# Optimization experiments

Measured on AMD Instinct MI355X. Metric: run time of the kernel, lower is better.

The kernel has to match this reference:

```python
import jax, jax.numpy as jnp
import numpy as np


def _gru_layer(x, w_ih, w_hh, b_ih, b_hh):
    """PyTorch-semantics GRU over x:[B,T,I]. w_ih:[3H,I], w_hh:[3H,H]."""
    B, T, I = x.shape
    H = w_hh.shape[1]
    # precompute input-side gates for all timesteps: [T,B,3H]
    gx = (jnp.einsum('bti,gi->btg', x, w_ih) + b_ih).transpose(1, 0, 2)

    def step(h, gx_t):
        gh = h @ w_hh.T + b_hh  # [B,3H]
        xr, xz, xn = jnp.split(gx_t, 3, axis=-1)
        hr, hz, hn = jnp.split(gh, 3, axis=-1)
        r = jax.nn.sigmoid(xr + hr)
        z = jax.nn.sigmoid(xz + hz)
        n = jnp.tanh(xn + r * hn)
        h_new = (1.0 - z) * n + z * h
        return h_new, h_new

    h0 = jnp.zeros((B, H), dtype=x.dtype)
    _, hs = jax.lax.scan(step, h0, gx)  # hs: [T,B,H]
    return hs.transpose(1, 0, 2)


def _gru_params(key, in_size, hidden):
    k = 1.0 / np.sqrt(hidden)
    k1, k2, k3, k4 = jax.random.split(key, 4)
    w_ih = jax.random.uniform(k1, (3 * hidden, in_size), minval=-k, maxval=k, dtype=jnp.float32)
    w_hh = jax.random.uniform(k2, (3 * hidden, hidden), minval=-k, maxval=k, dtype=jnp.float32)
    b_ih = jax.random.uniform(k3, (3 * hidden,), minval=-k, maxval=k, dtype=jnp.float32)
    b_hh = jax.random.uniform(k4, (3 * hidden,), minval=-k, maxval=k, dtype=jnp.float32)
    return w_ih, w_hh, b_ih, b_hh


def setup_inputs() -> dict:
    key = jax.random.key(0)
    ks = jax.random.split(key, 6)
    B, T = 256, 1024
    x = jax.random.normal(ks[0], (B, T), dtype=jnp.float32)
    sizes = [(1, 256), (256, 128), (128, 128), (128, 256)]
    d = {'x': x}
    for i, (isz, h) in enumerate(sizes):
        w_ih, w_hh, b_ih, b_hh = _gru_params(ks[1 + i], isz, h)
        d[f'w_ih{i+1}'] = w_ih
        d[f'w_hh{i+1}'] = w_hh
        d[f'b_ih{i+1}'] = b_ih
        d[f'b_hh{i+1}'] = b_hh
    kw, kb = jax.random.split(ks[5])
    kk = 1.0 / np.sqrt(256.0)
    d['w_out'] = jax.random.uniform(kw, (1, 256), minval=-kk, maxval=kk, dtype=jnp.float32)
    d['b_out'] = jax.random.uniform(kb, (1,), minval=-kk, maxval=kk, dtype=jnp.float32)
    return d


def reference(x, w_ih1, w_hh1, b_ih1, b_hh1,
              w_ih2, w_hh2, b_ih2, b_hh2,
              w_ih3, w_hh3, b_ih3, b_hh3,
              w_ih4, w_hh4, b_ih4, b_hh4,
              w_out, b_out):
    h = x[..., None]  # [B,T,1]
    h = _gru_layer(h, w_ih1, w_hh1, b_ih1, b_hh1)
    h = _gru_layer(h, w_ih2, w_hh2, b_ih2, b_hh2)
    h = _gru_layer(h, w_ih3, w_hh3, b_ih3, b_hh3)
    h = _gru_layer(h, w_ih4, w_hh4, b_ih4, b_hh4)
    y = jnp.einsum('bth,oh->bto', h, w_out) + b_out  # TimeDistributed Linear(256,1)
    return y.reshape(y.shape[0], -1)  # flatten from dim 1 -> [B,T]
```

## Files before the change

### kernel.cpp

```cpp
#include <hip/hip_runtime.h>
#include <math.h>


__device__ __forceinline__ float sigmoidf_(float v) {
    return 1.0f / (1.0f + __expf(-v));
}
__device__ __forceinline__ float tanhf_(float v) {
    float e = __expf(2.0f * v);
    return 1.0f - 2.0f / (e + 1.0f);
}

__global__ void prep_k(const float* __restrict__ src, float* __restrict__ dst,
                       int H, int J) {
    int idx = blockIdx.x * 256 + threadIdx.x;
    int total = 3 * H * J;
    if (idx < total) {
        int g = idx / (H * J);
        int rem = idx - g * H * J;
        int u = rem / J;
        int j = rem - u * J;
        dst[(u * 3 + g) * J + j] = src[(g * H + u) * J + j];
    }
}


__device__ __forceinline__ void flag_st(int* p, int v) {
    __hip_atomic_store(p, v, __ATOMIC_RELAXED, __HIP_MEMORY_SCOPE_AGENT);
}
__device__ __forceinline__ int flag_ld(const int* p) {
    return __hip_atomic_load(p, __ATOMIC_RELAXED, __HIP_MEMORY_SCOPE_AGENT);
}
__device__ __forceinline__ void ex_store(float* p, float v) {
    __hip_atomic_store(p, v, __ATOMIC_RELAXED, __HIP_MEMORY_SCOPE_AGENT);
}

__device__ __forceinline__ void pollw(const int* p, int tgt, bool active,
                                      int& fc) {
    bool need = active && (fc < tgt);
    if (!__any(need)) return;
    int spins = 0;
    while (true) {
        if (need) { fc = flag_ld(p); need = (fc < tgt); }
        if (!__any(need)) return;
        if (++spins > 16) __builtin_amdgcn_s_sleep(1);
        if (spins > 200000) return;
    }
}


template <int J>
__device__ __forceinline__ void stage_load(float4* r, const float* src) {
    constexpr int NF4 = (32 * J) / 1024;
    #pragma unroll
    for (int k = 0; k < NF4; ++k) {
        const float* p = src + (size_t)(k * 256 + threadIdx.x) * 4;
        asm volatile("global_load_dwordx4 %0, %1, off sc0 sc1"
                     : "=v"(r[k]) : "v"(p) : "memory");
    }
}

template <int J>
__device__ __forceinline__ void stage_write(const float4* r, float* dst) {
    constexpr int NF4 = (32 * J) / 1024;
    constexpr int LJ = (J == 256) ? 8 : 7;
    #pragma unroll
    for (int k = 0; k < NF4; ++k) {
        int i = (k * 256 + threadIdx.x) * 4;
        int b = i >> LJ;
        int j = i & (J - 1);
        *(float4*)(dst + b * (J + 4) + j) = r[k];
    }
}

template <int J>
__device__ __forceinline__ void stageX(float* dst, const float* src) {
    float4 tmp[(32 * J) / 1024];
    stage_load<J>(tmp, src);
    asm volatile("s_waitcnt vmcnt(0)" ::: "memory");
    stage_write<J>(tmp, dst);
}

template <int J>
__device__ __forceinline__ void zero32(float* dst) {
    for (int i = threadIdx.x; i < 32 * (J + 4); i += 256) dst[i] = 0.0f;
}

template <int U, int J>
__device__ __forceinline__ void ring_store(float* hout, const float* hst) {
    constexpr int LU = (U == 32) ? 5 : 4;
    #pragma unroll
    for (int k = 0; k < (32 * U) / 256; ++k) {
        int i = k * 256 + threadIdx.x;
        int b = i >> LU;
        int c = i & (U - 1);
        ex_store(hout + b * J + c, hst[b * (U + 4) + c]);
    }
}

template <int KB, int J>
__device__ __forceinline__ void dot3(const float* __restrict__ w3,
                                     const float* __restrict__ hst, int b0,
                                     float* ar, float* az, float* ac) {
    const float4* wr = (const float4*)w3;
    const float4* wz = (const float4*)(w3 + J);
    const float4* wn = (const float4*)(w3 + 2 * J);
    const float* rows[KB];
    #pragma unroll
    for (int k = 0; k < KB; ++k) rows[k] = hst + (b0 + k * (32 / KB)) * (J + 4);
    #pragma unroll 4
    for (int j4 = 0; j4 < J / 4; ++j4) {
        float4 a = wr[j4];
        float4 c = wz[j4];
        float4 d = wn[j4];
        #pragma unroll
        for (int k = 0; k < KB; ++k) {
            float4 hv = *(const float4*)(rows[k] + j4 * 4);
            ar[k] = fmaf(hv.x, a.x, ar[k]); ar[k] = fmaf(hv.y, a.y, ar[k]);
            ar[k] = fmaf(hv.z, a.z, ar[k]); ar[k] = fmaf(hv.w, a.w, ar[k]);
            az[k] = fmaf(hv.x, c.x, az[k]); az[k] = fmaf(hv.y, c.y, az[k]);
            az[k] = fmaf(hv.z, c.z, az[k]); az[k] = fmaf(hv.w, c.w, az[k]);
            ac[k] = fmaf(hv.x, d.x, ac[k]); ac[k] = fmaf(hv.y, d.y, ac[k]);
            ac[k] = fmaf(hv.z, d.z, ac[k]); ac[k] = fmaf(hv.w, d.w, ac[k]);
        }
    }
}

__global__ __launch_bounds__(256) void gru_pipe_kernel(
    const float* __restrict__ x,
    const float* __restrict__ w_ih1,
    const float* __restrict__ b_ih1, const float* __restrict__ b_hh1,
    const float* __restrict__ b_ih2, const float* __restrict__ b_hh2,
    const float* __restrict__ b_ih3, const float* __restrict__ b_hh3,
    const float* __restrict__ b_ih4, const float* __restrict__ b_hh4,
    const float* __restrict__ wA_hh1,
    const float* __restrict__ wA_ih2,
    const float* __restrict__ wA_hh2,
    const float* __restrict__ wA_ih3,
    const float* __restrict__ wA_hh3,
    const float* __restrict__ wA_ih4,
    const float* __restrict__ wA_hh4,
    const float* __restrict__ w_out, const float* __restrict__ b_out,
    int* __restrict__ flags,
    float* __restrict__ ex,
    float* __restrict__ out)
{
    const int tid = threadIdx.x;
    const int lane = tid & 63;
    extern __shared__ float smem[];
    __shared__ float xs[32];
    __shared__ float wsum[4][4][8];

    const int bg = blockIdx.x & 7;
    const int rest = blockIdx.x >> 3;
    const int s = rest >> 3;
    const int us = rest & 7;

    int* fb = flags + bg * 128;
    int* arr_own = fb + s * 32;

    const int* pT = arr_own; int dT = 0; bool aT = false;
    const int* pM = arr_own; bool aM = false;
    if (lane < 8) {
        if (s > 0) { pT = fb + (s - 1) * 32 + lane; dT = 1; aT = true; }
        pM = arr_own + lane; aM = true;
    } else if (lane < 16) {
        if (s < 3) { pT = fb + (s + 1) * 32 + (lane - 8); dT = -3; aT = true; }
    }
    const bool aUp = (s > 0) && (lane < 8);
    int fcT = 0, fcM = 0;

    float* exb = ex + (size_t)bg * 98304;
    float* h1r = exb;
    float* h2r = exb + 32768;
    float* h3r = exb + 49152;
    float* h4r = exb + 65536;

    if (s == 0) {
        float* wlds = smem;
        float* hprev = smem + 24704;
        float* hst = smem + 33024;
        {
            const float* srcw = wA_hh1 + (size_t)us * 32 * 768;
            for (int i = tid; i < 24576; i += 256) {
                int uu = i / 768, r = i - uu * 768;
                wlds[uu * 772 + r] = srcw[i];
            }
        }
        __syncthreads();
        const int ul = tid >> 3, b0 = tid & 7;
        const int u = us * 32 + ul;
        const float* wh = wlds + ul * 772;
        const float br = b_ih1[u] + b_hh1[u];
        const float bz = b_ih1[u + 256] + b_hh1[u + 256];
        const float bxn = b_ih1[u + 512];
        const float bhn = b_hh1[u + 512];
        const float wir = w_ih1[u], wiz = w_ih1[u + 256], win = w_ih1[u + 512];
        for (int t = 0; t < 1024; ++t) {
            pollw(pT, t + dT, aT, fcT);
            if (tid < 32) xs[tid] = x[(size_t)(bg * 32 + tid) * 1024 + t];
            pollw(pM, t, aM, fcM);
            if (t > 0) stageX<256>(hprev, h1r + (size_t)((t - 1) & 3) * 8192);
            else       zero32<256>(hprev);
            __syncthreads();
            float ar[4], az[4], axn[4], ahn[4];
            #pragma unroll
            for (int k = 0; k < 4; ++k) {
                float xv = xs[b0 + 8 * k];
                ar[k] = br + xv * wir; az[k] = bz + xv * wiz;
                axn[k] = bxn + xv * win; ahn[k] = bhn;
            }
            dot3<4, 256>(wh, hprev, b0, ar, az, ahn);
            float* hout = h1r + (size_t)(t & 3) * 8192;
            #pragma unroll
            for (int k = 0; k < 4; ++k) {
                int b = b0 + 8 * k;
                float hp = hprev[b * 260 + u];
                float r = sigmoidf_(ar[k]);
                float z = sigmoidf_(az[k]);
                float n = tanhf_(axn[k] + r * ahn[k]);
                hst[b * 36 + ul] = (1.f - z) * n + z * hp;
            }
            __syncthreads();
            ring_store<32, 256>(hout + us * 32, hst);
            asm volatile("s_waitcnt vmcnt(0)" ::: "memory");
            __syncthreads();
            if (tid == 0) flag_st(arr_own + us, t + 1);
        }
    } else if (s == 1) {
        float* wlds = smem;
        float* hin = smem + 6208;
        float* hprev = smem + 14528;
        float* hst = smem + 18752;
        {
            const float* srcw = wA_hh2 + (size_t)us * 16 * 384;
            for (int i = tid; i < 6144; i += 256) {
                int uu = i / 384, r = i - uu * 384;
                wlds[uu * 388 + r] = srcw[i];
            }
        }
        __syncthreads();
        const int ul = tid >> 4, b0 = tid & 15;
        const int u = us * 16 + ul;
        const float* wi = wA_ih2 + (size_t)u * 768;
        const float* wh = wlds + ul * 388;
        const float br = b_ih2[u] + b_hh2[u];
        const float bz = b_ih2[u + 128] + b_hh2[u + 128];
        const float bxn = b_ih2[u + 256];
        const float bhn = b_hh2[u + 256];
        float4 pregs[8];
        bool pf = false;
        for (int t = 0; t < 1024; ++t) {
            pollw(pT, t + dT, aT && (lane >= 8 || !pf), fcT);
            if (pf) stage_write<256>(pregs, hin);
            else    stageX<256>(hin, h1r + (size_t)(t & 3) * 8192);
            __syncthreads();
            float ar[2] = {br, br}, az[2] = {bz, bz};
            float axn[2] = {bxn, bxn}, ahn[2] = {bhn, bhn};
            dot3<2, 256>(wi, hin, b0, ar, az, axn);
            pollw(pM, t, aM, fcM);
            if (t > 0) stageX<128>(hprev, h2r + (size_t)((t - 1) & 3) * 4096);
            else       zero32<128>(hprev);
            __syncthreads();
            dot3<2, 128>(wh, hprev, b0, ar, az, ahn);
            pf = false;
            if (t < 1023) {
                if (aUp && fcT < t + 2) fcT = flag_ld(pT);
                pf = __all(!aUp || fcT >= t + 2);
                if (pf) stage_load<256>(pregs, h1r + (size_t)((t + 1) & 3) * 8192);
            }
            float* hout = h2r + (size_t)(t & 3) * 4096;
            #pragma unroll
            for (int k = 0; k < 2; ++k) {
                int b = b0 + 16 * k;
                float hp = hprev[b * 132 + u];
                float r = sigmoidf_(ar[k]);
                float z = sigmoidf_(az[k]);
                float n = tanhf_(axn[k] + r * ahn[k]);
                hst[b * 20 + ul] = (1.f - z) * n + z * hp;
            }
            __syncthreads();
            ring_store<16, 128>(hout + us * 16, hst);
            asm volatile("s_waitcnt vmcnt(0)" ::: "memory");
            __syncthreads();
            if (tid == 0) flag_st(arr_own + us, t + 1);
        }
    } else if (s == 2) {
        float* wlds = smem;
        float* hin = smem + 6208;
        float* hprev = smem + 10432;
        float* hst = smem + 14656;
        {
            const float* srcw = wA_hh3 + (size_t)us * 16 * 384;
            for (int i = tid; i < 6144; i += 256) {
                int uu = i / 384, r = i - uu * 384;
                wlds[uu * 388 + r] = srcw[i];
            }
        }
        __syncthreads();
        const int ul = tid >> 4, b0 = tid & 15;
        const int u = us * 16 + ul;
        const float* wi = wA_ih3 + (size_t)u * 384;
        const float* wh = wlds + ul * 388;
        const float br = b_ih3[u] + b_hh3[u];
        const float bz = b_ih3[u + 128] + b_hh3[u + 128];
        const float bxn = b_ih3[u + 256];
        const float bhn = b_hh3[u + 256];
        float4 pregs[4];
        bool pf = false;
        for (int t = 0; t < 1024; ++t) {
            pollw(pT, t + dT, aT && (lane >= 8 || !pf), fcT);
            if (pf) stage_write<128>(pregs, hin);
            else    stageX<128>(hin, h2r + (size_t)(t & 3) * 4096);
            __syncthreads();
            float ar[2] = {br, br}, az[2] = {bz, bz};
            float axn[2] = {bxn, bxn}, ahn[2] = {bhn, bhn};
            dot3<2, 128>(wi, hin, b0, ar, az, axn);
            pollw(pM, t, aM, fcM);
            if (t > 0) stageX<128>(hprev, h3r + (size_t)((t - 1) & 3) * 4096);
            else       zero32<128>(hprev);
            __syncthreads();
            dot3<2, 128>(wh, hprev, b0, ar, az, ahn);
            pf = false;
            if (t < 1023) {
                if (aUp && fcT < t + 2) fcT = flag_ld(pT);
                pf = __all(!aUp || fcT >= t + 2);
                if (pf) stage_load<128>(pregs, h2r + (size_t)((t + 1) & 3) * 4096);
            }
            float* hout = h3r + (size_t)(t & 3) * 4096;
            #pragma unroll
            for (int k = 0; k < 2; ++k) {
                int b = b0 + 16 * k;
                float hp = hprev[b * 132 + u];
                float r = sigmoidf_(ar[k]);
                float z = sigmoidf_(az[k]);
                float n = tanhf_(axn[k] + r * ahn[k]);
                hst[b * 20 + ul] = (1.f - z) * n + z * hp;
            }
            __syncthreads();
            ring_store<16, 128>(hout + us * 16, hst);
            asm volatile("s_waitcnt vmcnt(0)" ::: "memory");
            __syncthreads();
            if (tid == 0) flag_st(arr_own + us, t + 1);
        }
    } else {
        float* wlds = smem;
        float* hin = smem + 24704;
        float* hprev = smem + 28928;
        float* hst = smem + 37248;
        {
            const float* srcw = wA_hh4 + (size_t)us * 32 * 768;
            for (int i = tid; i < 24576; i += 256) {
                int uu = i / 768, r = i - uu * 768;
                wlds[uu * 772 + r] = srcw[i];
            }
        }
        __syncthreads();
        const int ul = tid >> 3, b0 = tid & 7;
        const int u = us * 32 + ul;
        const float* wi = wA_ih4 + (size_t)u * 384;
        const float* wh = wlds + ul * 772;
        const float br = b_ih4[u] + b_hh4[u];
        const float bz = b_ih4[u + 256] + b_hh4[u + 256];
        const float bxn = b_ih4[u + 512];
        const float bhn = b_hh4[u + 512];
        const float wo = w_out[u];
        float4 pregs[4];
        bool pf = false;
        for (int t = 0; t < 1024; ++t) {
            pollw(pT, t + dT, aT && !pf, fcT);
            if (pf) stage_write<128>(pregs, hin);
            else    stageX<128>(hin, h3r + (size_t)(t & 3) * 4096);
            __syncthreads();
            float ar[4], az[4], axn[4], ahn[4];
            #pragma unroll
            for (int k = 0; k < 4; ++k) {
                ar[k] = br; az[k] = bz; axn[k] = bxn; ahn[k] = bhn;
            }
            dot3<4, 128>(wi, hin, b0, ar, az, axn);
            pollw(pM, t, aM, fcM);
            if (t > 0) stageX<256>(hprev, h4r + (size_t)((t - 1) & 3) * 8192);
            else       zero32<256>(hprev);
            __syncthreads();
            dot3<4, 256>(wh, hprev, b0, ar, az, ahn);
            pf = false;
            if (t < 1023) {
                if (aUp && fcT < t + 2) fcT = flag_ld(pT);
                pf = __all(!aUp || fcT >= t + 2);
                if (pf) stage_load<128>(pregs, h3r + (size_t)((t + 1) & 3) * 4096);
            }
            float* hout = h4r + (size_t)(t & 3) * 8192;
            float pk[4];
            #pragma unroll
            for (int k = 0; k < 4; ++k) {
                int b = b0 + 8 * k;
                float hp = hprev[b * 260 + u];
                float r = sigmoidf_(ar[k]);
                float z = sigmoidf_(az[k]);
                float n = tanhf_(axn[k] + r * ahn[k]);
                float hnew = (1.f - z) * n + z * hp;
                hst[b * 36 + ul] = hnew;
                pk[k] = wo * hnew;
            }
            #pragma unroll
            for (int k = 0; k < 4; ++k) {
                pk[k] += __shfl_xor(pk[k], 8, 64);
                pk[k] += __shfl_xor(pk[k], 16, 64);
                pk[k] += __shfl_xor(pk[k], 32, 64);
            }
            if ((tid & 63) < 8) {
                int w = tid >> 6;
                #pragma unroll
                for (int k = 0; k < 4; ++k) wsum[w][k][tid & 7] = pk[k];
            }
            __syncthreads();
            ring_store<32, 256>(hout + us * 32, hst);
            asm volatile("s_waitcnt vmcnt(0)" ::: "memory");
            __syncthreads();
            if (tid == 0) flag_st(arr_own + us, t + 1);
            if (tid < 32) {
                int k = tid >> 3, bb = tid & 7;
                float ssum = wsum[0][k][bb] + wsum[1][k][bb] +
                             wsum[2][k][bb] + wsum[3][k][bb];
                if (us == 0) ssum += b_out[0];
                atomicAdd(out + (size_t)(bg * 32 + bb + 8 * k) * 1024 + t, ssum);
            }
        }
    }
}

extern "C" void kernel_launch(void* const* d_in, const int* in_sizes, int n_in,
                              void* d_out, int out_size, void* d_ws, size_t ws_size,
                              hipStream_t stream) {
    const float* x     = (const float*)d_in[0];
    const float* w_ih1 = (const float*)d_in[1];
    const float* w_hh1 = (const float*)d_in[2];
    const float* b_ih1 = (const float*)d_in[3];
    const float* b_hh1 = (const float*)d_in[4];
    const float* w_ih2 = (const float*)d_in[5];
    const float* w_hh2 = (const float*)d_in[6];
    const float* b_ih2 = (const float*)d_in[7];
    const float* b_hh2 = (const float*)d_in[8];
    const float* w_ih3 = (const float*)d_in[9];
    const float* w_hh3 = (const float*)d_in[10];
    const float* b_ih3 = (const float*)d_in[11];
    const float* b_hh3 = (const float*)d_in[12];
    const float* w_ih4 = (const float*)d_in[13];
    const float* w_hh4 = (const float*)d_in[14];
    const float* b_ih4 = (const float*)d_in[15];
    const float* b_hh4 = (const float*)d_in[16];
    const float* w_out = (const float*)d_in[17];
    const float* b_out = (const float*)d_in[18];

    float* ws = (float*)d_ws;
    float* wA_hh1 = ws;
    float* wA_ih2 = wA_hh1 + 196608;
    float* wA_hh2 = wA_ih2 + 98304;
    float* wA_ih3 = wA_hh2 + 49152;
    float* wA_hh3 = wA_ih3 + 49152;
    float* wA_ih4 = wA_hh3 + 49152;
    float* wA_hh4 = wA_ih4 + 98304;
    float* ex     = wA_hh4 + 196608;
    int*   flags  = (int*)(ex + 786432);

    (void)hipMemsetAsync(flags, 0, 1024 * sizeof(int), stream);
    (void)hipMemsetAsync(d_out, 0, 256 * 1024 * sizeof(float), stream);

    prep_k<<<768, 256, 0, stream>>>(w_hh1, wA_hh1, 256, 256);
    prep_k<<<384, 256, 0, stream>>>(w_ih2, wA_ih2, 128, 256);
    prep_k<<<192, 256, 0, stream>>>(w_hh2, wA_hh2, 128, 128);
    prep_k<<<192, 256, 0, stream>>>(w_ih3, wA_ih3, 128, 128);
    prep_k<<<192, 256, 0, stream>>>(w_hh3, wA_hh3, 128, 128);
    prep_k<<<384, 256, 0, stream>>>(w_ih4, wA_ih4, 256, 128);
    prep_k<<<768, 256, 0, stream>>>(w_hh4, wA_hh4, 256, 256);

    const int dyn_lds = 38400 * (int)sizeof(float);
    (void)hipFuncSetAttribute((const void*)gru_pipe_kernel,
                              hipFuncAttributeMaxDynamicSharedMemorySize, dyn_lds);

    gru_pipe_kernel<<<256, 256, dyn_lds, stream>>>(
        x, w_ih1, b_ih1, b_hh1, b_ih2, b_hh2, b_ih3, b_hh3, b_ih4, b_hh4,
        wA_hh1, wA_ih2, wA_hh2, wA_ih3, wA_hh3, wA_ih4, wA_hh4,
        w_out, b_out, flags, ex, (float*)d_out);
}
```

Measured before the change: 19.55 ms.

## Store hidden state directly to ring and prefetch flags earlier to shorten step latency

Each stage now writes its new hidden values straight to the global exchange ring instead of staging them in LDS, a barrier, and a coalesced ring_store. Flag loads for the upstream and downstream dependencies are issued early and their values reused, so later polls can often skip spinning. The next-step input prefetch now starts before the recurrent dot product rather than after it. The spin loop sleeps on every iteration. The trade-off is less coalesced, scattered atomic stores and a possibly slower reaction when a flag flips.

```diff
diff --git a/kernel.cpp b/kernel.cpp
--- a/kernel.cpp
+++ b/kernel.cpp
@@ -42,8 +42,8 @@
     while (true) {
         if (need) { fc = flag_ld(p); need = (fc < tgt); }
         if (!__any(need)) return;
-        if (++spins > 16) __builtin_amdgcn_s_sleep(1);
-        if (spins > 200000) return;
+        if (++spins > 200000) return;
+        __builtin_amdgcn_s_sleep(1);
     }
 }
 
@@ -83,18 +83,6 @@
 template <int J>
 __device__ __forceinline__ void zero32(float* dst) {
     for (int i = threadIdx.x; i < 32 * (J + 4); i += 256) dst[i] = 0.0f;
-}
-
-template <int U, int J>
-__device__ __forceinline__ void ring_store(float* hout, const float* hst) {
-    constexpr int LU = (U == 32) ? 5 : 4;
-    #pragma unroll
-    for (int k = 0; k < (32 * U) / 256; ++k) {
-        int i = k * 256 + threadIdx.x;
-        int b = i >> LU;
-        int c = i & (U - 1);
-        ex_store(hout + b * J + c, hst[b * (U + 4) + c]);
-    }
 }
 
 template <int KB, int J>
@@ -178,7 +166,6 @@
     if (s == 0) {
         float* wlds = smem;
         float* hprev = smem + 24704;
-        float* hst = smem + 33024;
         {
             const float* srcw = wA_hh1 + (size_t)us * 32 * 768;
             for (int i = tid; i < 24576; i += 256) {
@@ -195,13 +182,16 @@
         const float bxn = b_ih1[u + 512];
         const float bhn = b_hh1[u + 512];
         const float wir = w_ih1[u], wiz = w_ih1[u + 256], win = w_ih1[u + 512];
+        int freshM = 0;
         for (int t = 0; t < 1024; ++t) {
             pollw(pT, t + dT, aT, fcT);
             if (tid < 32) xs[tid] = x[(size_t)(bg * 32 + tid) * 1024 + t];
+            if (aM && freshM > fcM) fcM = freshM;
             pollw(pM, t, aM, fcM);
             if (t > 0) stageX<256>(hprev, h1r + (size_t)((t - 1) & 3) * 8192);
             else       zero32<256>(hprev);
             __syncthreads();
+            int freshT = aT ? flag_ld(pT) : 0;
             float ar[4], az[4], axn[4], ahn[4];
             #pragma unroll
             for (int k = 0; k < 4; ++k) {
@@ -218,19 +208,18 @@
                 float r = sigmoidf_(ar[k]);
                 float z = sigmoidf_(az[k]);
                 float n = tanhf_(axn[k] + r * ahn[k]);
-                hst[b * 36 + ul] = (1.f - z) * n + z * hp;
-            }
-            __syncthreads();
-            ring_store<32, 256>(hout + us * 32, hst);
+                ex_store(hout + b * 256 + u, (1.f - z) * n + z * hp);
+            }
+            if (aT && freshT > fcT) fcT = freshT;
             asm volatile("s_waitcnt vmcnt(0)" ::: "memory");
             __syncthreads();
             if (tid == 0) flag_st(arr_own + us, t + 1);
+            freshM = aM ? flag_ld(pM) : 0;
         }
     } else if (s == 1) {
         float* wlds = smem;
         float* hin = smem + 6208;
         float* hprev = smem + 14528;
-        float* hst = smem + 18752;
         {
             const float* srcw = wA_hh2 + (size_t)us * 16 * 384;
             for (int i = tid; i < 6144; i += 256) {
@@ -254,20 +243,22 @@
             if (pf) stage_write<256>(pregs, hin);
             else    stageX<256>(hin, h1r + (size_t)(t & 3) * 8192);
             __syncthreads();
+            int freshM = aM ? flag_ld(pM) : 0;
             float ar[2] = {br, br}, az[2] = {bz, bz};
             float axn[2] = {bxn, bxn}, ahn[2] = {bhn, bhn};
             dot3<2, 256>(wi, hin, b0, ar, az, axn);
+            bool pf_n = false;
+            if (t < 1023) {
+                pf_n = __all(!aUp || fcT >= t + 2);
+                if (pf_n) stage_load<256>(pregs, h1r + (size_t)((t + 1) & 3) * 8192);
+            }
+            int freshT = aT ? flag_ld(pT) : 0;
+            if (aM && freshM > fcM) fcM = freshM;
             pollw(pM, t, aM, fcM);
             if (t > 0) stageX<128>(hprev, h2r + (size_t)((t - 1) & 3) * 4096);
             else       zero32<128>(hprev);
             __syncthreads();
             dot3<2, 128>(wh, hprev, b0, ar, az, ahn);
-            pf = false;
-            if (t < 1023) {
-                if (aUp && fcT < t + 2) fcT = flag_ld(pT);
-                pf = __all(!aUp || fcT >= t + 2);
-                if (pf) stage_load<256>(pregs, h1r + (size_t)((t + 1) & 3) * 8192);
-            }
             float* hout = h2r + (size_t)(t & 3) * 4096;
             #pragma unroll
             for (int k = 0; k < 2; ++k) {
@@ -276,10 +267,10 @@
                 float r = sigmoidf_(ar[k]);
                 float z = sigmoidf_(az[k]);
                 float n = tanhf_(axn[k] + r * ahn[k]);
-                hst[b * 20 + ul] = (1.f - z) * n + z * hp;
-            }
-            __syncthreads();
-            ring_store<16, 128>(hout + us * 16, hst);
+                ex_store(hout + b * 128 + u, (1.f - z) * n + z * hp);
+            }
+            if (aT && freshT > fcT) fcT = freshT;
+            pf = pf_n;
             asm volatile("s_waitcnt vmcnt(0)" ::: "memory");
             __syncthreads();
             if (tid == 0) flag_st(arr_own + us, t + 1);
@@ -288,7 +279,6 @@
         float* wlds = smem;
         float* hin = smem + 6208;
         float* hprev = smem + 10432;
-        float* hst = smem + 14656;
         {
             const float* srcw = wA_hh3 + (size_t)us * 16 * 384;
             for (int i = tid; i < 6144; i += 256) {
@@ -312,20 +302,22 @@
             if (pf) stage_write<128>(pregs, hin);
             else    stageX<128>(hin, h2r + (size_t)(t & 3) * 4096);
             __syncthreads();
+            int freshM = aM ? flag_ld(pM) : 0;
             float ar[2] = {br, br}, az[2] = {bz, bz};
             float axn[2] = {bxn, bxn}, ahn[2] = {bhn, bhn};
             dot3<2, 128>(wi, hin, b0, ar, az, axn);
+            bool pf_n = false;
+            if (t < 1023) {
+                pf_n = __all(!aUp || fcT >= t + 2);
+                if (pf_n) stage_load<128>(pregs, h2r + (size_t)((t + 1) & 3) * 4096);
+            }
+            int freshT = aT ? flag_ld(pT) : 0;
+            if (aM && freshM > fcM) fcM = freshM;
             pollw(pM, t, aM, fcM);
             if (t > 0) stageX<128>(hprev, h3r + (size_t)((t - 1) & 3) * 4096);
             else       zero32<128>(hprev);
             __syncthreads();
             dot3<2, 128>(wh, hprev, b0, ar, az, ahn);
-            pf = false;
-            if (t < 1023) {
-                if (aUp && fcT < t + 2) fcT = flag_ld(pT);
-                pf = __all(!aUp || fcT >= t + 2);
-                if (pf) stage_load<128>(pregs, h2r + (size_t)((t + 1) & 3) * 4096);
-            }
             float* hout = h3r + (size_t)(t & 3) * 4096;
             #pragma unroll
             for (int k = 0; k < 2; ++k) {
@@ -334,10 +326,10 @@
                 float r = sigmoidf_(ar[k]);
                 float z = sigmoidf_(az[k]);
                 float n = tanhf_(axn[k] + r * ahn[k]);
-                hst[b * 20 + ul] = (1.f - z) * n + z * hp;
-            }
-            __syncthreads();
-            ring_store<16, 128>(hout + us * 16, hst);
+                ex_store(hout + b * 128 + u, (1.f - z) * n + z * hp);
+            }
+            if (aT && freshT > fcT) fcT = freshT;
+            pf = pf_n;
             asm volatile("s_waitcnt vmcnt(0)" ::: "memory");
             __syncthreads();
             if (tid == 0) flag_st(arr_own + us, t + 1);
@@ -346,7 +338,6 @@
         float* wlds = smem;
         float* hin = smem + 24704;
         float* hprev = smem + 28928;
-        float* hst = smem + 37248;
         {
             const float* srcw = wA_hh4 + (size_t)us * 32 * 768;
             for (int i = tid; i < 24576; i += 256) {
@@ -371,23 +362,25 @@
             if (pf) stage_write<128>(pregs, hin);
             else    stageX<128>(hin, h3r + (size_t)(t & 3) * 4096);
             __syncthreads();
+            int freshM = aM ? flag_ld(pM) : 0;
             float ar[4], az[4], axn[4], ahn[4];
             #pragma unroll
             for (int k = 0; k < 4; ++k) {
                 ar[k] = br; az[k] = bz; axn[k] = bxn; ahn[k] = bhn;
             }
             dot3<4, 128>(wi, hin, b0, ar, az, axn);
+            bool pf_n = false;
+            if (t < 1023) {
+                pf_n = __all(!aUp || fcT >= t + 2);
+                if (pf_n) stage_load<128>(pregs, h3r + (size_t)((t + 1) & 3) * 4096);
+            }
+            int freshT = aT ? flag_ld(pT) : 0;
+            if (aM && freshM > fcM) fcM = freshM;
             pollw(pM, t, aM, fcM);
             if (t > 0) stageX<256>(hprev, h4r + (size_t)((t - 1) & 3) * 8192);
             else       zero32<256>(hprev);
             __syncthreads();
             dot3<4, 256>(wh, hprev, b0, ar, az, ahn);
-            pf = false;
-            if (t < 1023) {
-                if (aUp && fcT < t + 2) fcT = flag_ld(pT);
-                pf = __all(!aUp || fcT >= t + 2);
-                if (pf) stage_load<128>(pregs, h3r + (size_t)((t + 1) & 3) * 4096);
-            }
             float* hout = h4r + (size_t)(t & 3) * 8192;
             float pk[4];
             #pragma unroll
@@ -398,7 +391,7 @@
                 float z = sigmoidf_(az[k]);
                 float n = tanhf_(axn[k] + r * ahn[k]);
                 float hnew = (1.f - z) * n + z * hp;
-                hst[b * 36 + ul] = hnew;
+                ex_store(hout + b * 256 + u, hnew);
                 pk[k] = wo * hnew;
             }
             #pragma unroll
@@ -412,8 +405,8 @@
                 #pragma unroll
                 for (int k = 0; k < 4; ++k) wsum[w][k][tid & 7] = pk[k];
             }
-            __syncthreads();
-            ring_store<32, 256>(hout + us * 32, hst);
+            if (aT && freshT > fcT) fcT = freshT;
+            pf = pf_n;
             asm volatile("s_waitcnt vmcnt(0)" ::: "memory");
             __syncthreads();
             if (tid == 0) flag_st(arr_own + us, t + 1);
@@ -473,7 +466,7 @@
     prep_k<<<384, 256, 0, stream>>>(w_ih4, wA_ih4, 256, 128);
     prep_k<<<768, 256, 0, stream>>>(w_hh4, wA_hh4, 256, 256);
 
-    const int dyn_lds = 38400 * (int)sizeof(float);
+    const int dyn_lds = 37248 * (int)sizeof(float);
     (void)hipFuncSetAttribute((const void*)gru_pipe_kernel,
                               hipFuncAttributeMaxDynamicSharedMemorySize, dyn_lds);
 
```

Result: faster. 18.91 ms (-3.2%).
